# Kernel optimization log

Hardware: AMD Instinct MI355X
Metric: run time of the kernel (lower is better)

Reference implementation:

```python
import jax, jax.numpy as jnp
import numpy as np

N_NODES = 100000
N_EDGES = 1600000
N_PAIRS = 200000
IN_C, HID_C, EMB_C, PRED_H = 128, 128, 64, 256


def setup_inputs() -> dict:
    key = jax.random.key(0)
    ks = jax.random.split(key, 12)
    glorot = lambda k, fi, fo: jax.random.normal(k, (fi, fo), jnp.float32) * (2.0 / (fi + fo)) ** 0.5
    return {
        "x": jax.random.normal(ks[0], (N_NODES, IN_C), jnp.float32),
        "edge_index": jax.random.randint(ks[1], (2, N_EDGES), 0, N_NODES, jnp.int64 if jax.config.jax_enable_x64 else jnp.int32),
        "edge_label_index": jax.random.randint(ks[2], (2, N_PAIRS), 0, N_NODES, jnp.int64 if jax.config.jax_enable_x64 else jnp.int32),
        "W1": glorot(ks[3], IN_C, HID_C),
        "b1": jnp.zeros((HID_C,), jnp.float32),
        "W2": glorot(ks[4], HID_C, EMB_C),
        "b2": jnp.zeros((EMB_C,), jnp.float32),
        "Wm1": glorot(ks[5], 4 * EMB_C, PRED_H),
        "bm1": jnp.zeros((PRED_H,), jnp.float32),
        "Wm2": glorot(ks[6], PRED_H, 1),
        "bm2": jnpp if False else jnp.zeros((1,), jnp.float32),
    }


def _gcn_conv(x, W, b, src, dst, n):
    # x: [N, Fin]; src/dst: [E+N] (self-loops included)
    h = x @ W                                              # [N, Fout]
    deg = jax.ops.segment_sum(jnp.ones_like(dst, dtype=h.dtype), dst, num_segments=n)
    dinv = jnp.where(deg > 0, jax.lax.rsqrt(deg), 0.0)     # deg^{-1/2}
    coef = (dinv[src] * dinv[dst])[:, None]                # symmetric norm per edge
    out = jax.ops.segment_sum(h[src] * coef, dst, num_segments=n)
    return out + b


def reference(x, edge_index, edge_label_index, W1, b1, W2, b2, Wm1, bm1, Wm2, bm2):
    n = x.shape[0]
    loop = jnp.arange(n, dtype=edge_index.dtype)
    src = jnp.concatenate([edge_index[0], loop])           # add self-loops (PyG GCNConv default)
    dst = jnp.concatenate([edge_index[1], loop])
    h = jax.nn.relu(_gcn_conv(x, W1, b1, src, dst, n))     # conv1 + relu (dropout p=0/eval)
    z = _gcn_conv(h, W2, b2, src, dst, n)                  # conv2 -> [N, EMB_C]
    zs = z[edge_label_index[0]]                            # [P, EMB_C]
    zd = z[edge_label_index[1]]
    pf = jnp.concatenate([zs, zd, zs * zd, jnp.abs(zs - zd)], axis=-1)  # [P, 4*EMB_C]
    hm = jax.nn.relu(pf @ Wm1 + bm1)
    logits = (hm @ Wm2 + bm2).reshape(-1)                  # [P]
    return logits
```

## Files before the change

### kernel.cpp

```cpp
#include <hip/hip_runtime.h>
#include <hip/hip_bf16.h>
#include <hip/hip_fp16.h>

#define NODES 100000
#define INC 128
#define HIDC 128
#define EMBC 64
#define PREDH 256

#define BSH 9
#define BNODES (1 << BSH)
#define MTILE 8192

typedef __attribute__((ext_vector_type(8))) _Float16 half8;
typedef __attribute__((ext_vector_type(4))) float f32x4;

__global__ void k_deg(const int* __restrict__ ei, int* __restrict__ deg, int E) {
    int e = blockIdx.x * 256 + threadIdx.x;
    if (e >= E) return;
    atomicAdd(&deg[ei[E + e]], 1);
}

__global__ __launch_bounds__(1024) void k_scan1(const int* __restrict__ deg,
                                                int* __restrict__ rowptr,
                                                int* __restrict__ bsum, int n) {
    __shared__ int tmp[1024];
    int tid = threadIdx.x;
    int i = blockIdx.x * 1024 + tid;
    int v = (i < n) ? deg[i] : 0;
    tmp[tid] = v;
    __syncthreads();
    for (int off = 1; off < 1024; off <<= 1) {
        int t = (tid >= off) ? tmp[tid - off] : 0;
        __syncthreads();
        tmp[tid] += t;
        __syncthreads();
    }
    if (i < n) rowptr[i] = tmp[tid] - v;
    if (tid == 1023) bsum[blockIdx.x] = tmp[1023];
}

__global__ __launch_bounds__(128) void k_scan2(int* __restrict__ bsum, int nb) {
    __shared__ int tmp[128];
    int tid = threadIdx.x;
    int v = (tid < nb) ? bsum[tid] : 0;
    tmp[tid] = v;
    __syncthreads();
    for (int off = 1; off < 128; off <<= 1) {
        int t = (tid >= off) ? tmp[tid - off] : 0;
        __syncthreads();
        tmp[tid] += t;
        __syncthreads();
    }
    if (tid < nb) bsum[tid] = tmp[tid] - v;
}

__global__ __launch_bounds__(1024) void k_scan3(int* __restrict__ rowptr,
                                                const int* __restrict__ bsum,
                                                const int* __restrict__ deg,
                                                float* __restrict__ dinv,
                                                int* __restrict__ gcur, int n) {
    int i = blockIdx.x * 1024 + threadIdx.x;
    if (i >= n) return;
    int r = rowptr[i] + bsum[blockIdx.x];
    rowptr[i] = r;
    dinv[i] = rsqrtf((float)(deg[i] + 1));
    if ((i & (BNODES - 1)) == 0) gcur[i >> BSH] = r;
}

template <int NB>
__global__ __launch_bounds__(256) void k_msplit(const int* __restrict__ ei,
                                                int* __restrict__ gcur,
                                                unsigned* __restrict__ ebuf, int E) {
    __shared__ int lcnt[NB];
    __shared__ int lbase[NB];
    int tid = threadIdx.x;
    int t0 = blockIdx.x * MTILE;
    int iend = min(t0 + MTILE, E);
    for (int i = tid; i < NB; i += 256) lcnt[i] = 0;
    __syncthreads();
    for (int i = t0 + tid; i < iend; i += 256)
        atomicAdd(&lcnt[ei[E + i] >> BSH], 1);
    __syncthreads();
    for (int i = tid; i < NB; i += 256) {
        int c = lcnt[i];
        lbase[i] = c ? atomicAdd(&gcur[i], c) : 0;
        lcnt[i] = 0;
    }
    __syncthreads();
    for (int i = t0 + tid; i < iend; i += 256) {
        int s = ei[i], d = ei[E + i];
        int b = d >> BSH;
        int r = atomicAdd(&lcnt[b], 1);
        ebuf[lbase[b] + r] = ((unsigned)s << BSH) | (unsigned)(d & (BNODES - 1));
    }
}

__global__ __launch_bounds__(256) void k_csrB(const unsigned* __restrict__ ebuf,
                                              const int* __restrict__ rowptr,
                                              int* __restrict__ col, int n, int E) {
    __shared__ int curs[BNODES];
    int b = blockIdx.x;
    int node0 = b << BSH;
    int tid = threadIdx.x;
    for (int i = tid; i < BNODES; i += 256) {
        int nd = node0 + i;
        curs[i] = (nd < n) ? rowptr[nd] : 0;
    }
    int start = rowptr[node0];
    int end = (node0 + BNODES < n) ? rowptr[node0 + BNODES] : E;
    __syncthreads();
    for (int i = start + tid; i < end; i += 256) {
        unsigned v = ebuf[i];
        int pos = atomicAdd(&curs[v & (unsigned)(BNODES - 1)], 1);
        col[pos] = (int)(v >> BSH);
    }
}

__global__ void k_prepall(const float* __restrict__ Wm1, const float* __restrict__ W1,
                          const float* __restrict__ W2, _Float16* __restrict__ WmT,
                          _Float16* __restrict__ W1T, _Float16* __restrict__ W2T) {
    int i = blockIdx.x * 256 + threadIdx.x;
    if (i < 256 * 256) {
        int nn = i >> 8, kk = i & 255;
        WmT[i] = (_Float16)Wm1[kk * 256 + nn];
    } else if (i < 256 * 256 + 128 * 128) {
        int j = i - 256 * 256;
        int nn = j >> 7, kk = j & 127;
        W1T[j] = (_Float16)W1[kk * 128 + nn];
    } else if (i < 256 * 256 + 128 * 128 + 64 * 128) {
        int j = i - 256 * 256 - 128 * 128;
        int nn = j >> 7, kk = j & 127;
        W2T[j] = (_Float16)W2[kk * 64 + nn];
    }
}

template <int N, int K, bool XF32>
__global__ __launch_bounds__(256) void k_mmf(const void* __restrict__ Xv,
                                             const _Float16* __restrict__ WT,
                                             const float* __restrict__ dinv,
                                             _Float16* __restrict__ O, int M) {
    int tid = threadIdx.x;
    int wid = tid >> 6, lane = tid & 63;
    int lr = lane & 15, kg = lane >> 4;
    int row0 = blockIdx.x * 64 + wid * 16;
    int arow = min(row0 + lr, M - 1);
    const int NF = N / 16;
    f32x4 acc[NF];
#pragma unroll
    for (int nr = 0; nr < NF; nr++) acc[nr] = (f32x4){0.f, 0.f, 0.f, 0.f};

#pragma unroll
    for (int ks = 0; ks < K / 32; ks++) {
        half8 a;
        if (XF32) {
            const float* Xf = (const float*)Xv + (size_t)arow * K + ks * 32 + kg * 8;
            float4 x0 = *(const float4*)Xf;
            float4 x1 = *(const float4*)(Xf + 4);
            a[0] = (_Float16)x0.x; a[1] = (_Float16)x0.y;
            a[2] = (_Float16)x0.z; a[3] = (_Float16)x0.w;
            a[4] = (_Float16)x1.x; a[5] = (_Float16)x1.y;
            a[6] = (_Float16)x1.z; a[7] = (_Float16)x1.w;
        } else {
            a = *(const half8*)((const _Float16*)Xv + (size_t)arow * K + ks * 32 + kg * 8);
        }
#pragma unroll
        for (int nr = 0; nr < NF; nr++) {
            half8 b = *(const half8*)&WT[(size_t)(nr * 16 + lr) * K + ks * 32 + kg * 8];
            acc[nr] = __builtin_amdgcn_mfma_f32_16x16x32_f16(a, b, acc[nr], 0, 0, 0);
        }
    }

    int orow0 = row0 + kg * 4;
    float dv[4];
#pragma unroll
    for (int r = 0; r < 4; r++) dv[r] = dinv[min(orow0 + r, M - 1)];
#pragma unroll
    for (int nr = 0; nr < NF; nr++)
#pragma unroll
        for (int r = 0; r < 4; r++) {
            int orow = orow0 + r;
            if (orow < M)
                O[(size_t)orow * N + nr * 16 + lr] = (_Float16)(acc[nr][r] * dv[r]);
        }
}

template <int C, bool RELU>
__global__ __launch_bounds__(256) void k_gath(const _Float16* __restrict__ Hs,
                                              const float* __restrict__ dinv,
                                              const int* __restrict__ rowptr,
                                              const int* __restrict__ deg,
                                              const int* __restrict__ col,
                                              const float* __restrict__ b,
                                              _Float16* __restrict__ O, int n) {
    const int LPR = C / 8;
    const int EPI = 64 / LPR;
    int wid = threadIdx.x >> 6;
    int node = blockIdx.x * 4 + wid;
    if (node >= n) return;
    int lane = threadIdx.x & 63;
    int grp = lane / LPR;
    int lane2 = lane % LPR;
    int start = rowptr[node];
    int cnt = deg[node];
    float dd = dinv[node];

    float acc[8] = {0.f, 0.f, 0.f, 0.f, 0.f, 0.f, 0.f, 0.f};
    for (int j = 0; j < cnt; j += EPI) {
        int e = j + grp;
        if (e < cnt) {
            int s = col[start + e];
            half8 h = *(const half8*)&Hs[(size_t)s * C + lane2 * 8];
#pragma unroll
            for (int t = 0; t < 8; t++) acc[t] += (float)h[t];
        }
    }
#pragma unroll
    for (int t = 0; t < 8; t++) {
        float v = acc[t];
#pragma unroll
        for (int off = LPR; off < 64; off <<= 1)
            v += __shfl_xor(v, off);
        acc[t] = v;
    }
    if (grp == 0) {
        half8 hs = *(const half8*)&Hs[(size_t)node * C + lane2 * 8];
        const float* bp = b + lane2 * 8;
        half8 o;
#pragma unroll
        for (int t = 0; t < 8; t++) {
            float v = (acc[t] + (float)hs[t]) * dd + bp[t];
            if (RELU) v = fmaxf(v, 0.f);
            o[t] = (_Float16)v;
        }
        *(half8*)&O[(size_t)node * C + lane2 * 8] = o;
    }
}

__global__ __launch_bounds__(256) void k_predm(const _Float16* __restrict__ Z,
                                               const int* __restrict__ eli,
                                               const _Float16* __restrict__ WT,
                                               const float* __restrict__ bm1,
                                               const float* __restrict__ Wm2,
                                               const float* __restrict__ bm2,
                                               float* __restrict__ out, int P) {
    __shared__ _Float16 pf[64][264];
    __shared__ float red[4][64];
    int tid = threadIdx.x;
    int p0 = blockIdx.x * 64;

    {
        int pr = tid >> 2, q = tid & 3;
        int pg = p0 + pr;
        int s = 0, d = 0;
        if (pg < P) { s = eli[pg]; d = eli[P + pg]; }
        const half8* zs8 = (const half8*)(Z + (size_t)s * 64 + q * 16);
        const half8* zd8 = (const half8*)(Z + (size_t)d * 64 + q * 16);
#pragma unroll
        for (int h = 0; h < 2; ++h) {
            half8 za = zs8[h], zb = zd8[h];
            int c = q * 16 + h * 8;
#pragma unroll
            for (int t = 0; t < 8; ++t) {
                float a = (float)za[t], bb = (float)zb[t];
                pf[pr][c + t] = za[t];
                pf[pr][64 + c + t] = zb[t];
                pf[pr][128 + c + t] = (_Float16)(a * bb);
                pf[pr][192 + c + t] = (_Float16)fabsf(a - bb);
            }
        }
    }
    __syncthreads();

    int wid = tid >> 6, lane = tid & 63;
    int lr = lane & 15, kg = lane >> 4;
    int n0 = wid * 64;

    float wmv[4], bmv[4];
#pragma unroll
    for (int nr = 0; nr < 4; nr++) {
        int nn = n0 + nr * 16 + lr;
        wmv[nr] = Wm2[nn];
        bmv[nr] = bm1[nn];
    }

    f32x4 acc[4][4];
#pragma unroll
    for (int mr = 0; mr < 4; mr++)
#pragma unroll
        for (int nr = 0; nr < 4; nr++) acc[mr][nr] = (f32x4){0.f, 0.f, 0.f, 0.f};

    for (int ks = 0; ks < 8; ks++) {
        half8 a[4], b[4];
#pragma unroll
        for (int mr = 0; mr < 4; mr++)
            a[mr] = *(const half8*)&pf[mr * 16 + lr][ks * 32 + kg * 8];
#pragma unroll
        for (int nr = 0; nr < 4; nr++)
            b[nr] = *(const half8*)&WT[(size_t)(n0 + nr * 16 + lr) * 256 + ks * 32 + kg * 8];
#pragma unroll
        for (int mr = 0; mr < 4; mr++)
#pragma unroll
            for (int nr = 0; nr < 4; nr++)
                acc[mr][nr] = __builtin_amdgcn_mfma_f32_16x16x32_f16(a[mr], b[nr], acc[mr][nr], 0, 0, 0);
    }

#pragma unroll
    for (int mr = 0; mr < 4; mr++) {
#pragma unroll
        for (int reg = 0; reg < 4; reg++) {
            float p = 0.f;
#pragma unroll
            for (int nr = 0; nr < 4; nr++)
                p += fmaxf(acc[mr][nr][reg] + bmv[nr], 0.f) * wmv[nr];
            p += __shfl_xor(p, 1);
            p += __shfl_xor(p, 2);
            p += __shfl_xor(p, 4);
            p += __shfl_xor(p, 8);
            if (lr == 0) red[wid][mr * 16 + kg * 4 + reg] = p;
        }
    }
    __syncthreads();
    if (tid < 64) {
        int pg = p0 + tid;
        if (pg < P)
            out[pg] = red[0][tid] + red[1][tid] + red[2][tid] + red[3][tid] + bm2[0];
    }
}

extern "C" void kernel_launch(void* const* d_in, const int* in_sizes, int n_in,
                              void* d_out, int out_size, void* d_ws, size_t ws_size,
                              hipStream_t stream) {
    const float* x   = (const float*)d_in[0];
    const int*   ei  = (const int*)d_in[1];
    const int*   eli = (const int*)d_in[2];
    const float* W1  = (const float*)d_in[3];
    const float* b1  = (const float*)d_in[4];
    const float* W2  = (const float*)d_in[5];
    const float* b2  = (const float*)d_in[6];
    const float* Wm1 = (const float*)d_in[7];
    const float* bm1 = (const float*)d_in[8];
    const float* Wm2 = (const float*)d_in[9];
    const float* bm2 = (const float*)d_in[10];
    float* out = (float*)d_out;

    const int n = NODES;
    const int E = in_sizes[1] / 2;
    const int P = in_sizes[2] / 2;
    const int NB = (n + BNODES - 1) / BNODES;

    char* ws = (char*)d_ws;
    size_t off = 0;
    auto alloc = [&](size_t bytes) {
        size_t o = off;
        off += (bytes + 255) & ~(size_t)255;
        return o;
    };
    int*      deg    = (int*)(ws + alloc((size_t)n * 4));
    int*      rowptr = (int*)(ws + alloc((size_t)n * 4));
    int*      gcur   = (int*)(ws + alloc(512 * 4));
    unsigned* ebuf   = (unsigned*)(ws + alloc((size_t)E * 4));
    int*      colx   = (int*)(ws + alloc((size_t)E * 4));
    int*      bsum   = (int*)(ws + alloc(512 * 4));
    float*    dinv   = (float*)(ws + alloc((size_t)n * 4));
    _Float16* WmT    = (_Float16*)(ws + alloc((size_t)256 * 256 * 2));
    _Float16* W1T    = (_Float16*)(ws + alloc((size_t)128 * 128 * 2));
    _Float16* W2T    = (_Float16*)(ws + alloc((size_t)64 * 128 * 2));
    _Float16* Hs1    = (_Float16*)(ws + alloc((size_t)n * HIDC * 2));
    _Float16* C1     = (_Float16*)(ws + alloc((size_t)n * HIDC * 2));
    _Float16* Hs2    = (_Float16*)(ws + alloc((size_t)n * EMBC * 2));
    _Float16* Z      = (_Float16*)(ws + alloc((size_t)n * EMBC * 2));

    hipMemsetAsync(deg, 0, (size_t)n * 4, stream);
    k_deg<<<(E + 255) / 256, 256, 0, stream>>>(ei, deg, E);
    {
        int tot = 256 * 256 + 128 * 128 + 64 * 128;
        k_prepall<<<(tot + 255) / 256, 256, 0, stream>>>(Wm1, W1, W2, WmT, W1T, W2T);
    }
    int nb = (n + 1023) / 1024;
    k_scan1<<<nb, 1024, 0, stream>>>(deg, rowptr, bsum, n);
    k_scan2<<<1, 128, 0, stream>>>(bsum, nb);
    k_scan3<<<nb, 1024, 0, stream>>>(rowptr, bsum, deg, dinv, gcur, n);
    k_msplit<196><<<(E + MTILE - 1) / MTILE, 256, 0, stream>>>(ei, gcur, ebuf, E);
    k_csrB<<<NB, 256, 0, stream>>>(ebuf, rowptr, colx, n, E);

    int mmGrid = (n + 63) / 64;

    k_mmf<HIDC, INC, true><<<mmGrid, 256, 0, stream>>>(x, W1T, dinv, Hs1, n);
    k_gath<HIDC, true><<<(n + 3) / 4, 256, 0, stream>>>(Hs1, dinv, rowptr, deg, colx, b1, C1, n);

    k_mmf<EMBC, HIDC, false><<<mmGrid, 256, 0, stream>>>(C1, W2T, dinv, Hs2, n);
    k_gath<EMBC, false><<<(n + 3) / 4, 256, 0, stream>>>(Hs2, dinv, rowptr, deg, colx, b2, Z, n);

    k_predm<<<(P + 63) / 64, 256, 0, stream>>>(Z, eli, WmT, bm1, Wm2, bm2, out, P);
}
```

Before: 459.3 us.

## Build CSR via bucket counts and per-bucket local scan; unroll gather loop

Replaces the global per-node degree atomics and the three-kernel node scan with a bucket-level count (shared-memory histogram), a single-block bucket scan, and a per-bucket local histogram plus scan inside the CSR build kernel. That kernel now produces rowptr, deg and dinv itself. This removes about 1.6M global atomics and several launches from the CSR build, at the cost of reading ebuf twice per bucket. It also unrolls the aggregation gather loop by two to keep more loads in flight.

```diff
diff --git a/kernel.cpp b/kernel.cpp
--- a/kernel.cpp
+++ b/kernel.cpp
@@ -15,57 +15,43 @@
 typedef __attribute__((ext_vector_type(8))) _Float16 half8;
 typedef __attribute__((ext_vector_type(4))) float f32x4;
 
-__global__ void k_deg(const int* __restrict__ ei, int* __restrict__ deg, int E) {
-    int e = blockIdx.x * 256 + threadIdx.x;
-    if (e >= E) return;
-    atomicAdd(&deg[ei[E + e]], 1);
-}
-
-__global__ __launch_bounds__(1024) void k_scan1(const int* __restrict__ deg,
-                                                int* __restrict__ rowptr,
-                                                int* __restrict__ bsum, int n) {
-    __shared__ int tmp[1024];
-    int tid = threadIdx.x;
-    int i = blockIdx.x * 1024 + tid;
-    int v = (i < n) ? deg[i] : 0;
+template <int NB>
+__global__ __launch_bounds__(256) void k_bcnt(const int* __restrict__ ei,
+                                              int* __restrict__ gcnt, int E) {
+    __shared__ int lcnt[NB];
+    int tid = threadIdx.x;
+    int t0 = blockIdx.x * MTILE;
+    int iend = min(t0 + MTILE, E);
+    for (int i = tid; i < NB; i += 256) lcnt[i] = 0;
+    __syncthreads();
+    for (int i = t0 + tid; i < iend; i += 256)
+        atomicAdd(&lcnt[ei[E + i] >> BSH], 1);
+    __syncthreads();
+    for (int i = tid; i < NB; i += 256)
+        if (lcnt[i]) atomicAdd(&gcnt[i], lcnt[i]);
+}
+
+template <int NB>
+__global__ __launch_bounds__(256) void k_bscan(const int* __restrict__ gcnt,
+                                               int* __restrict__ gbase,
+                                               int* __restrict__ gcur, int E) {
+    __shared__ int tmp[256];
+    int tid = threadIdx.x;
+    int v = (tid < NB) ? gcnt[tid] : 0;
     tmp[tid] = v;
     __syncthreads();
-    for (int off = 1; off < 1024; off <<= 1) {
+    for (int off = 1; off < 256; off <<= 1) {
         int t = (tid >= off) ? tmp[tid - off] : 0;
         __syncthreads();
         tmp[tid] += t;
         __syncthreads();
     }
-    if (i < n) rowptr[i] = tmp[tid] - v;
-    if (tid == 1023) bsum[blockIdx.x] = tmp[1023];
-}
-
-__global__ __launch_bounds__(128) void k_scan2(int* __restrict__ bsum, int nb) {
-    __shared__ int tmp[128];
-    int tid = threadIdx.x;
-    int v = (tid < nb) ? bsum[tid] : 0;
-    tmp[tid] = v;
-    __syncthreads();
-    for (int off = 1; off < 128; off <<= 1) {
-        int t = (tid >= off) ? tmp[tid - off] : 0;
-        __syncthreads();
-        tmp[tid] += t;
-        __syncthreads();
-    }
-    if (tid < nb) bsum[tid] = tmp[tid] - v;
-}
-
-__global__ __launch_bounds__(1024) void k_scan3(int* __restrict__ rowptr,
-                                                const int* __restrict__ bsum,
-                                                const int* __restrict__ deg,
-                                                float* __restrict__ dinv,
-                                                int* __restrict__ gcur, int n) {
-    int i = blockIdx.x * 1024 + threadIdx.x;
-    if (i >= n) return;
-    int r = rowptr[i] + bsum[blockIdx.x];
-    rowptr[i] = r;
-    dinv[i] = rsqrtf((float)(deg[i] + 1));
-    if ((i & (BNODES - 1)) == 0) gcur[i >> BSH] = r;
+    if (tid < NB) {
+        int e = tmp[tid] - v;
+        gbase[tid] = e;
+        gcur[tid] = e;
+    }
+    if (tid == NB) gbase[NB] = E;
 }
 
 template <int NB>
@@ -96,21 +82,48 @@
     }
 }
 
-__global__ __launch_bounds__(256) void k_csrB(const unsigned* __restrict__ ebuf,
-                                              const int* __restrict__ rowptr,
-                                              int* __restrict__ col, int n, int E) {
+__global__ __launch_bounds__(256) void k_csrB2(const unsigned* __restrict__ ebuf,
+                                               const int* __restrict__ gbase,
+                                               int* __restrict__ rowptr,
+                                               int* __restrict__ deg,
+                                               float* __restrict__ dinv,
+                                               int* __restrict__ col, int n) {
+    __shared__ int cnt[BNODES];
+    __shared__ int psum[256];
     __shared__ int curs[BNODES];
     int b = blockIdx.x;
+    int tid = threadIdx.x;
     int node0 = b << BSH;
-    int tid = threadIdx.x;
-    for (int i = tid; i < BNODES; i += 256) {
-        int nd = node0 + i;
-        curs[i] = (nd < n) ? rowptr[nd] : 0;
-    }
-    int start = rowptr[node0];
-    int end = (node0 + BNODES < n) ? rowptr[node0 + BNODES] : E;
-    __syncthreads();
-    for (int i = start + tid; i < end; i += 256) {
+    int base = gbase[b];
+    int end = gbase[b + 1];
+    cnt[2 * tid] = 0;
+    cnt[2 * tid + 1] = 0;
+    __syncthreads();
+    for (int i = base + tid; i < end; i += 256)
+        atomicAdd(&cnt[ebuf[i] & (unsigned)(BNODES - 1)], 1);
+    __syncthreads();
+    int a0 = cnt[2 * tid], a1 = cnt[2 * tid + 1];
+    int pair = a0 + a1;
+    psum[tid] = pair;
+    __syncthreads();
+    for (int off = 1; off < 256; off <<= 1) {
+        int t = (tid >= off) ? psum[tid - off] : 0;
+        __syncthreads();
+        psum[tid] += t;
+        __syncthreads();
+    }
+    int excl = psum[tid] - pair;
+    {
+        int g0 = base + excl;
+        int g1 = g0 + a0;
+        int nd0 = node0 + 2 * tid, nd1 = nd0 + 1;
+        if (nd0 < n) { rowptr[nd0] = g0; deg[nd0] = a0; dinv[nd0] = rsqrtf((float)(a0 + 1)); }
+        if (nd1 < n) { rowptr[nd1] = g1; deg[nd1] = a1; dinv[nd1] = rsqrtf((float)(a1 + 1)); }
+        curs[2 * tid] = g0;
+        curs[2 * tid + 1] = g1;
+    }
+    __syncthreads();
+    for (int i = base + tid; i < end; i += 256) {
         unsigned v = ebuf[i];
         int pos = atomicAdd(&curs[v & (unsigned)(BNODES - 1)], 1);
         col[pos] = (int)(v >> BSH);
@@ -206,7 +219,16 @@
     float dd = dinv[node];
 
     float acc[8] = {0.f, 0.f, 0.f, 0.f, 0.f, 0.f, 0.f, 0.f};
-    for (int j = 0; j < cnt; j += EPI) {
+    int j = 0;
+    for (; j + 2 * EPI <= cnt; j += 2 * EPI) {
+        int s0 = col[start + j + grp];
+        int s1 = col[start + j + EPI + grp];
+        half8 h0 = *(const half8*)&Hs[(size_t)s0 * C + lane2 * 8];
+        half8 h1 = *(const half8*)&Hs[(size_t)s1 * C + lane2 * 8];
+#pragma unroll
+        for (int t = 0; t < 8; t++) acc[t] += (float)h0[t] + (float)h1[t];
+    }
+    for (; j < cnt; j += EPI) {
         int e = j + grp;
         if (e < cnt) {
             int s = col[start + e];
@@ -358,10 +380,11 @@
     };
     int*      deg    = (int*)(ws + alloc((size_t)n * 4));
     int*      rowptr = (int*)(ws + alloc((size_t)n * 4));
+    int*      gcnt   = (int*)(ws + alloc(512 * 4));
+    int*      gbase  = (int*)(ws + alloc(512 * 4));
     int*      gcur   = (int*)(ws + alloc(512 * 4));
     unsigned* ebuf   = (unsigned*)(ws + alloc((size_t)E * 4));
     int*      colx   = (int*)(ws + alloc((size_t)E * 4));
-    int*      bsum   = (int*)(ws + alloc(512 * 4));
     float*    dinv   = (float*)(ws + alloc((size_t)n * 4));
     _Float16* WmT    = (_Float16*)(ws + alloc((size_t)256 * 256 * 2));
     _Float16* W1T    = (_Float16*)(ws + alloc((size_t)128 * 128 * 2));
@@ -371,18 +394,16 @@
     _Float16* Hs2    = (_Float16*)(ws + alloc((size_t)n * EMBC * 2));
     _Float16* Z      = (_Float16*)(ws + alloc((size_t)n * EMBC * 2));
 
-    hipMemsetAsync(deg, 0, (size_t)n * 4, stream);
-    k_deg<<<(E + 255) / 256, 256, 0, stream>>>(ei, deg, E);
+    hipMemsetAsync(gcnt, 0, 512 * 4, stream);
     {
         int tot = 256 * 256 + 128 * 128 + 64 * 128;
         k_prepall<<<(tot + 255) / 256, 256, 0, stream>>>(Wm1, W1, W2, WmT, W1T, W2T);
     }
-    int nb = (n + 1023) / 1024;
-    k_scan1<<<nb, 1024, 0, stream>>>(deg, rowptr, bsum, n);
-    k_scan2<<<1, 128, 0, stream>>>(bsum, nb);
-    k_scan3<<<nb, 1024, 0, stream>>>(rowptr, bsum, deg, dinv, gcur, n);
-    k_msplit<196><<<(E + MTILE - 1) / MTILE, 256, 0, stream>>>(ei, gcur, ebuf, E);
-    k_csrB<<<NB, 256, 0, stream>>>(ebuf, rowptr, colx, n, E);
+    int mgrid = (E + MTILE - 1) / MTILE;
+    k_bcnt<196><<<mgrid, 256, 0, stream>>>(ei, gcnt, E);
+    k_bscan<196><<<1, 256, 0, stream>>>(gcnt, gbase, gcur, E);
+    k_msplit<196><<<mgrid, 256, 0, stream>>>(ei, gcur, ebuf, E);
+    k_csrB2<<<NB, 256, 0, stream>>>(ebuf, gbase, rowptr, deg, dinv, colx, n);
 
     int mmGrid = (n + 63) / 64;
 
```

New measurement: 382.8 us. 1.2x faster.
